# Optimization experiments

Measured on AMD Instinct MI355X. Metric: run time of the kernel, lower is better.

## Reference

```python
import jax, jax.numpy as jnp
import numpy as np

# Per-chromosome bin counts: round(len/100000) for hg38 chromosome lengths (from __init__)
CHROM_BINS = [2490, 2422, 1983, 1902, 1815, 1708, 1593, 1451, 1384, 1338, 1351,
              1333, 1144, 1070, 1020, 903, 833, 804, 586, 644, 467, 508]
LOC = np.concatenate([[0], np.cumsum(CHROM_BINS)])  # 23 boundaries, LOC[-1] == 28749
TOTAL_BINS = int(LOC[-1])
COMP = 50          # compression_size
N_HEADS = 22
INPUT_DIM = N_HEADS * COMP * 2  # 2200
H1, H2, OUT = 1000, 50, 13
BATCH = 2048


def setup_inputs() -> dict:
    key = jax.random.key(0)
    ks = jax.random.split(key, 12)
    s = 0.02
    return {
        "input_tensor": jax.random.normal(ks[0], (BATCH, 2, TOTAL_BINS), jnp.float32),
        # all 22 head weight matrices concatenated along the input dim: (COMP, TOTAL_BINS)
        "head_w": jax.random.normal(ks[1], (COMP, TOTAL_BINS), jnp.float32) * s,
        "head_b": jax.random.normal(ks[2], (N_HEADS, COMP), jnp.float32) * s,
        "conc_w": jax.random.normal(ks[3], (INPUT_DIM, INPUT_DIM), jnp.float32) * s,
        "conc_b": jax.random.normal(ks[4], (INPUT_DIM,), jnp.float32) * s,
        "w1": jax.random.normal(ks[5], (H1, INPUT_DIM), jnp.float32) * s,
        "b1": jax.random.normal(ks[6], (H1,), jnp.float32) * s,
        "w2": jax.random.normal(ks[7], (H2, H1), jnp.float32) * s,
        "b2": jax.random.normal(ks[8], (H2,), jnp.float32) * s,
        "w3": jax.random.normal(ks[9], (OUT, H2), jnp.float32) * s,
        "b3": jax.random.normal(ks[10], (OUT,), jnp.float32) * s,
    }


def reference(input_tensor, head_w, head_b, conc_w, conc_b, w1, b1, w2, b2, w3, b3):
    # 22 per-chromosome heads, each applied to both channels; output order per
    # chromosome i is [head_i(ch0), head_i(ch1)], matching the torch loop.
    pieces = []
    for i in range(N_HEADS):
        a, b = int(LOC[i]), int(LOC[i + 1])
        seg = input_tensor[:, :, a:b]                       # (B, 2, L_i)
        h = jnp.einsum('bcl,ol->bco', seg, head_w[:, a:b]) + head_b[i]  # (B, 2, COMP)
        pieces.append(h.reshape(h.shape[0], -1))            # (B, 2*COMP)
    combined = jnp.concatenate(pieces, axis=1)              # (B, 2200)
    z = combined @ conc_w.T + conc_b                        # conc Linear
    # seq: Linear -> Dropout(eval=id) -> LeakyReLU -> Linear -> Dropout -> LeakyReLU -> Dropout -> Linear
    h1 = jax.nn.leaky_relu(z @ w1.T + b1, 0.01)
    h2 = jax.nn.leaky_relu(h1 @ w2.T + b2, 0.01)
    return h2 @ w3.T + b3                                   # (B, 13)
```

## Files before the change

kernel.cpp:

```cpp
#include <hip/hip_runtime.h>
#include <cstdint>

typedef __bf16 bf16_t;
typedef __bf16 bf16x4 __attribute__((ext_vector_type(4)));
typedef __bf16 bf16x8 __attribute__((ext_vector_type(8)));
typedef float  f32x4  __attribute__((ext_vector_type(4)));
typedef float  f32x4u __attribute__((ext_vector_type(4), aligned(4)));

#define TOTAL_BINS 28749
#define WH_LD64    29312
#define N_HEADS    22
#define BATCH      2048
#define ROWS       4096
#define IDIM       2200
#define IDIM_P     2208
#define IDIM_NP    2240
#define H1DIM      1000
#define H1_NP      1024
#define H2DIM      50
#define ODIM       13
#define KSPLIT     8

__constant__ int d_LOC[23]  = {0,2490,4912,6895,8797,10612,12320,13913,15364,16748,
                               18086,19437,20770,21914,22984,24004,24907,25740,26544,
                               27130,27774,28241,28749};
__constant__ int d_HA64[23] = {0,2496,4928,6912,8832,10688,12416,14016,15488,16896,
                               18240,19648,20992,22144,23232,24256,25216,26112,26944,
                               27584,28288,28800,29312};

__device__ __forceinline__ void g2lds16(const void* g, void* l) {
  __builtin_amdgcn_global_load_lds((const __attribute__((address_space(1))) void*)g,
                                   (__attribute__((address_space(3))) void*)l, 16, 0, 0);
}

__device__ __forceinline__ f32x4 mfma16(bf16x8 a, bf16x8 b, f32x4 c) {
  return __builtin_amdgcn_mfma_f32_16x16x32_bf16(a, b, c, 0, 0, 0);
}

__global__ __launch_bounds__(256) void convert_pad8(const float* __restrict__ src,
                                                    bf16_t* __restrict__ dst,
                                                    int rows, int cols, int prow, int pcol)
{
  size_t i = (size_t)blockIdx.x * 256 + threadIdx.x;
  int pc8 = pcol >> 3;
  if (i >= (size_t)prow * pc8) return;
  int r  = (int)(i / pc8);
  int c0 = (int)(i - (size_t)r * pc8) * 8;
  bf16x8 o;
  if (r < rows && c0 + 8 <= cols) {
    f32x4u a = *(const f32x4u*)(src + (size_t)r * cols + c0);
    f32x4u b = *(const f32x4u*)(src + (size_t)r * cols + c0 + 4);
    #pragma unroll
    for (int j = 0; j < 4; j++) { o[j] = (bf16_t)a[j]; o[4 + j] = (bf16_t)b[j]; }
  } else {
    #pragma unroll
    for (int j = 0; j < 8; j++) {
      int c = c0 + j;
      o[j] = (bf16_t)((r < rows && c < cols) ? src[(size_t)r * cols + c] : 0.0f);
    }
  }
  *(bf16x8*)(dst + (size_t)r * pcol + c0) = o;
}

__global__ __launch_bounds__(256) void convert_headw8(const float* __restrict__ src,
                                                      bf16_t* __restrict__ dst)
{
  size_t i = (size_t)blockIdx.x * 256 + threadIdx.x;
  const int pc8 = WH_LD64 / 8;
  if (i >= (size_t)64 * pc8) return;
  int r  = (int)(i / pc8);
  int c0 = (int)(i - (size_t)r * pc8) * 8;
  int head = 0;
  #pragma unroll
  for (int h = 0; h < N_HEADS; h++) if (c0 >= d_HA64[h + 1]) head = h + 1;
  const int ha = d_HA64[head], a = d_LOC[head];
  const int L  = d_LOC[head + 1] - a;
  const int k0 = c0 - ha;
  bf16x8 o;
  if (r < 50 && k0 + 8 <= L) {
    const float* s = src + (size_t)r * TOTAL_BINS + a + k0;
    f32x4u x = *(const f32x4u*)(s);
    f32x4u y = *(const f32x4u*)(s + 4);
    #pragma unroll
    for (int j = 0; j < 4; j++) { o[j] = (bf16_t)x[j]; o[4 + j] = (bf16_t)y[j]; }
  } else {
    #pragma unroll
    for (int j = 0; j < 8; j++) {
      int k = k0 + j;
      o[j] = (bf16_t)((r < 50 && k < L) ? src[(size_t)r * TOTAL_BINS + a + k] : 0.0f);
    }
  }
  *(bf16x8*)(dst + (size_t)r * WH_LD64 + c0) = o;
}

__global__ __launch_bounds__(256) void head_gemm2(const float* __restrict__ X,
                                                  const bf16_t* __restrict__ Wh,
                                                  const float* __restrict__ headb,
                                                  bf16_t* __restrict__ Cmb)
{
  __shared__ __attribute__((aligned(16))) bf16_t Ws[2][64][72];
  const int tid = threadIdx.x, lane = tid & 63, wid = tid >> 6;
  const int head = blockIdx.y;
  const int a   = d_LOC[head];
  const int ha  = d_HA64[head];
  const int L64 = d_HA64[head + 1] - ha;
  const int m0  = blockIdx.x * 64;
  const int la = lane & 15, lk = lane >> 4;
  const int wrow = m0 + wid * 16 + la;
  const uint32_t rowbase = (uint32_t)wrow * TOTAL_BINS + (uint32_t)a;
  const uint32_t MAX4 = (uint32_t)ROWS * TOTAL_BINS - 4;

  const int sn = tid >> 2, skg = (tid & 3) * 16;
  const bf16_t* wsrc = Wh + (size_t)sn * WH_LD64 + ha + skg;

  f32x4 acc[4] = {};

  #define LOADA(dst, kbase) do {                                     \
    uint32_t b0_ = (kbase) + (uint32_t)(lk * 8);                     \
    dst[0] = *(const f32x4u*)(X + min(b0_,      MAX4));              \
    dst[1] = *(const f32x4u*)(X + min(b0_ + 4,  MAX4));              \
    dst[2] = *(const f32x4u*)(X + min(b0_ + 32, MAX4));              \
    dst[3] = *(const f32x4u*)(X + min(b0_ + 36, MAX4));              \
  } while (0)

  {
    uint4 w0 = *(const uint4*)(wsrc);
    uint4 w1 = *(const uint4*)(wsrc + 8);
    *(uint4*)(&Ws[0][sn][skg])     = w0;
    *(uint4*)(&Ws[0][sn][skg + 8]) = w1;
  }
  f32x4u ar[4];
  LOADA(ar, rowbase);

  const int nIter = L64 >> 6;
  for (int i = 0; i < nIter; i++) {
    __syncthreads();
    const int cur = i & 1, nxt = cur ^ 1;
    uint4 nw0, nw1; f32x4u an[4];
    const bool more = (i + 1 < nIter);
    if (more) {
      const bf16_t* ws2 = wsrc + (size_t)(i + 1) * 64;
      nw0 = *(const uint4*)(ws2);
      nw1 = *(const uint4*)(ws2 + 8);
      LOADA(an, rowbase + (uint32_t)(i + 1) * 64);
    }
    bf16x8 af[2];
    #pragma unroll
    for (int kq = 0; kq < 2; kq++)
      #pragma unroll
      for (int j = 0; j < 8; j++)
        af[kq][j] = (bf16_t)ar[kq * 2 + (j >> 2)][j & 3];
    #pragma unroll
    for (int kq = 0; kq < 2; kq++)
      #pragma unroll
      for (int j = 0; j < 4; j++) {
        bf16x8 bf = *(const bf16x8*)(&Ws[cur][j * 16 + la][kq * 32 + lk * 8]);
        acc[j] = mfma16(af[kq], bf, acc[j]);
      }
    if (more) {
      *(uint4*)(&Ws[nxt][sn][skg])     = nw0;
      *(uint4*)(&Ws[nxt][sn][skg + 8]) = nw1;
      #pragma unroll
      for (int q = 0; q < 4; q++) ar[q] = an[q];
    }
  }

  #pragma unroll
  for (int j = 0; j < 4; j++) {
    int o = j * 16 + la;
    if (o < 50) {
      float bv = headb[head * 50 + o];
      #pragma unroll
      for (int r = 0; r < 4; r++) {
        int gr = m0 + wid * 16 + lk * 4 + r;
        Cmb[(size_t)(gr >> 1) * IDIM_P + head * 100 + (gr & 1) * 50 + o] =
            (bf16_t)(acc[j][r] + bv);
      }
    }
  }
  #undef LOADA
}

__global__ __launch_bounds__(256) void gemm_bt64(const bf16_t* __restrict__ A, int lda,
                                                 const bf16_t* __restrict__ W, int ldb,
                                                 const float* __restrict__ bias,
                                                 void* __restrict__ Cout, int ldc,
                                                 int K, int N, int act, int out_f32)
{
  __shared__ __attribute__((aligned(16))) bf16_t As[2][128][32];
  __shared__ __attribute__((aligned(16))) bf16_t Bs[2][64][32];
  const int tid  = threadIdx.x;
  const int lane = tid & 63, wid = tid >> 6;
  const int m0 = blockIdx.x * 128;
  const int n0 = blockIdx.y * 64;
  const int la = lane & 15, lk = lane >> 4;
  const int wm = wid * 32;
  const int scg = (((tid & 3) ^ ((tid >> 3) & 3)) * 8);
  const int lks = ((lk ^ ((la >> 1) & 3)) * 8);

  f32x4 acc[2][4] = {};

  const bf16_t* asrc0 = A + (size_t)(m0 + (tid >> 2)) * lda + scg;
  const bf16_t* asrc1 = asrc0 + (size_t)64 * lda;
  const bf16_t* wsrc  = W + (size_t)(n0 + (tid >> 2)) * ldb + scg;

  auto stage = [&](int buf, int k0) {
    g2lds16(asrc0 + k0, &As[buf][0][0] + tid * 8);
    g2lds16(asrc1 + k0, &As[buf][64][0] + tid * 8);
    g2lds16(wsrc  + k0, &Bs[buf][0][0] + tid * 8);
  };
  stage(0, 0);

  int i = 0;
  for (int k0 = 0; k0 < K; k0 += 32, i++) {
    __syncthreads();
    const int cur = i & 1;
    if (k0 + 32 < K) stage(cur ^ 1, k0 + 32);
    bf16x8 af[2], bfr[4];
    #pragma unroll
    for (int ii = 0; ii < 2; ii++) af[ii]  = *(const bf16x8*)(&As[cur][wm + ii * 16 + la][lks]);
    #pragma unroll
    for (int j = 0; j < 4; j++)    bfr[j] = *(const bf16x8*)(&Bs[cur][j * 16 + la][lks]);
    #pragma unroll
    for (int ii = 0; ii < 2; ii++)
      #pragma unroll
      for (int j = 0; j < 4; j++)
        acc[ii][j] = mfma16(af[ii], bfr[j], acc[ii][j]);
  }

  float bv[4]; bool ok[4]; int gcv[4];
  #pragma unroll
  for (int j = 0; j < 4; j++) {
    int gc = n0 + j * 16 + la;
    gcv[j] = gc; ok[j] = gc < N;
    bv[j] = ok[j] ? bias[gc] : 0.0f;
  }
  #pragma unroll
  for (int ii = 0; ii < 2; ii++) {
    #pragma unroll
    for (int r = 0; r < 4; r++) {
      int gr = m0 + wm + ii * 16 + lk * 4 + r;
      #pragma unroll
      for (int j = 0; j < 4; j++) {
        if (ok[j]) {
          float v = acc[ii][j][r] + bv[j];
          if (act) v = fmaxf(v, 0.01f * v);
          if (out_f32) ((float*) Cout)[(size_t)gr * ldc + gcv[j]] = v;
          else         ((bf16_t*)Cout)[(size_t)gr * ldc + gcv[j]] = (bf16_t)v;
        }
      }
    }
  }
}

__global__ __launch_bounds__(256) void gemm_splitk(const bf16_t* __restrict__ A,
                                                   const bf16_t* __restrict__ W,
                                                   float* __restrict__ P)
{
  __shared__ __attribute__((aligned(16))) bf16_t As[2][128][32];
  __shared__ __attribute__((aligned(16))) bf16_t Bs[2][64][32];
  const int tid  = threadIdx.x;
  const int lane = tid & 63, wid = tid >> 6;
  const int m0 = blockIdx.x * 128;
  const int split = blockIdx.y;
  const int kb = split * (H1_NP / KSPLIT);
  const int la = lane & 15, lk = lane >> 4;
  const int wm = wid * 32;
  const int scg = (((tid & 3) ^ ((tid >> 3) & 3)) * 8);
  const int lks = ((lk ^ ((la >> 1) & 3)) * 8);

  f32x4 acc[2][4] = {};

  const bf16_t* asrc0 = A + (size_t)(m0 + (tid >> 2)) * H1_NP + kb + scg;
  const bf16_t* asrc1 = asrc0 + (size_t)64 * H1_NP;
  const bf16_t* wsrc  = W + (size_t)(tid >> 2) * H1_NP + kb + scg;

  auto stage = [&](int buf, int k0) {
    g2lds16(asrc0 + k0, &As[buf][0][0] + tid * 8);
    g2lds16(asrc1 + k0, &As[buf][64][0] + tid * 8);
    g2lds16(wsrc  + k0, &Bs[buf][0][0] + tid * 8);
  };
  stage(0, 0);

  #pragma unroll
  for (int i = 0; i < 4; i++) {
    __syncthreads();
    const int cur = i & 1;
    if (i < 3) stage(cur ^ 1, (i + 1) * 32);
    bf16x8 af[2], bfr[4];
    #pragma unroll
    for (int ii = 0; ii < 2; ii++) af[ii]  = *(const bf16x8*)(&As[cur][wm + ii * 16 + la][lks]);
    #pragma unroll
    for (int j = 0; j < 4; j++)    bfr[j] = *(const bf16x8*)(&Bs[cur][j * 16 + la][lks]);
    #pragma unroll
    for (int ii = 0; ii < 2; ii++)
      #pragma unroll
      for (int j = 0; j < 4; j++)
        acc[ii][j] = mfma16(af[ii], bfr[j], acc[ii][j]);
  }

  #pragma unroll
  for (int ii = 0; ii < 2; ii++)
    #pragma unroll
    for (int r = 0; r < 4; r++) {
      int gr = m0 + wm + ii * 16 + lk * 4 + r;
      #pragma unroll
      for (int j = 0; j < 4; j++)
        P[((size_t)split * BATCH + gr) * 64 + j * 16 + la] = acc[ii][j][r];
    }
}

__global__ __launch_bounds__(256) void finalize_tail(const float* __restrict__ P,
                                                     const float* __restrict__ b2,
                                                     const float* __restrict__ w3,
                                                     const float* __restrict__ b3,
                                                     float* __restrict__ out)
{
  __shared__ float h2s[16][64];
  const int r0 = blockIdx.x * 16;
  const int t = threadIdx.x;
  const int r = t >> 4, c4 = (t & 15) * 4;
  f32x4 s = {};
  #pragma unroll
  for (int sp = 0; sp < KSPLIT; sp++) {
    const f32x4 v = *(const f32x4*)(P + ((size_t)sp * BATCH + r0 + r) * 64 + c4);
    s.x += v.x; s.y += v.y; s.z += v.z; s.w += v.w;
  }
  #pragma unroll
  for (int c = 0; c < 4; c++) {
    int col = c4 + c;
    float v = s[c] + ((col < H2DIM) ? b2[col] : 0.0f);
    h2s[r][col] = fmaxf(v, 0.01f * v);
  }
  __syncthreads();
  if (t < 16 * ODIM) {
    int rr = t / ODIM, o = t - rr * ODIM;
    float acc = b3[o];
    #pragma unroll 10
    for (int k = 0; k < H2DIM; k++) acc += h2s[rr][k] * w3[o * H2DIM + k];
    out[(size_t)(r0 + rr) * ODIM + o] = acc;
  }
}

extern "C" void kernel_launch(void* const* d_in, const int* in_sizes, int n_in,
                              void* d_out, int out_size, void* d_ws, size_t ws_size,
                              hipStream_t stream)
{
  const float* X      = (const float*)d_in[0];
  const float* head_w = (const float*)d_in[1];
  const float* head_b = (const float*)d_in[2];
  const float* conc_w = (const float*)d_in[3];
  const float* conc_b = (const float*)d_in[4];
  const float* w1     = (const float*)d_in[5];
  const float* b1     = (const float*)d_in[6];
  const float* w2     = (const float*)d_in[7];
  const float* b2     = (const float*)d_in[8];
  const float* w3     = (const float*)d_in[9];
  const float* b3     = (const float*)d_in[10];

  char* p = (char*)d_ws;
  auto alloc = [&](size_t bytes) { char* r = p; p += (bytes + 255) & ~(size_t)255; return r; };
  bf16_t* headw_ws = (bf16_t*)alloc((size_t)64 * WH_LD64 * 2);
  bf16_t* concw_ws = (bf16_t*)alloc((size_t)IDIM_NP * IDIM_P * 2);
  bf16_t* w1_ws    = (bf16_t*)alloc((size_t)H1_NP * IDIM_P * 2);
  bf16_t* w2_ws    = (bf16_t*)alloc((size_t)128 * H1_NP * 2);
  bf16_t* comb     = (bf16_t*)alloc((size_t)BATCH * IDIM_P * 2);
  bf16_t* zbuf     = (bf16_t*)alloc((size_t)BATCH * IDIM_P * 2);
  bf16_t* h1buf    = (bf16_t*)alloc((size_t)BATCH * H1_NP * 2);
  float*  h2p      = (float*) alloc((size_t)KSPLIT * BATCH * 64 * 4);

  auto cgrid = [](size_t n) { return dim3((unsigned)((n + 255) / 256)); };

  convert_headw8<<<cgrid((size_t)64 * WH_LD64 / 8), 256, 0, stream>>>(head_w, headw_ws);
  convert_pad8<<<cgrid((size_t)IDIM_NP * IDIM_P / 8), 256, 0, stream>>>(conc_w, concw_ws, IDIM, IDIM, IDIM_NP, IDIM_P);
  convert_pad8<<<cgrid((size_t)H1_NP * IDIM_P / 8), 256, 0, stream>>>(w1, w1_ws, H1DIM, IDIM, H1_NP, IDIM_P);
  convert_pad8<<<cgrid((size_t)128 * H1_NP / 8), 256, 0, stream>>>(w2, w2_ws, H2DIM, H1DIM, 128, H1_NP);

  head_gemm2<<<dim3(ROWS / 64, N_HEADS), 256, 0, stream>>>(X, headw_ws, head_b, comb);

  gemm_bt64<<<dim3(BATCH / 128, IDIM_NP / 64), 256, 0, stream>>>(
      comb, IDIM_P, concw_ws, IDIM_P, conc_b, zbuf, IDIM_P, IDIM_P, IDIM, 0, 0);
  gemm_bt64<<<dim3(BATCH / 128, H1_NP / 64), 256, 0, stream>>>(
      zbuf, IDIM_P, w1_ws, IDIM_P, b1, h1buf, H1_NP, IDIM_P, H1DIM, 1, 0);

  gemm_splitk<<<dim3(BATCH / 128, KSPLIT), 256, 0, stream>>>(h1buf, w2_ws, h2p);
  finalize_tail<<<dim3(BATCH / 16), 256, 0, stream>>>(h2p, b2, w3, b3, (float*)d_out);
}
```

Before: 801.7 us.

## Fuse weight conversions, split-K the w1 GEMM, and remap workgroups across XCDs

Merges the four weight-conversion launches into one kernel that dispatches on block index, which cuts launch overhead. The w1 GEMM, which had only 256 blocks, now runs as a two-way split-K writing fp32 partials, and a new reduce kernel sums them and applies bias and LeakyReLU. Both GEMMs also remap the linear block index in an 8-way interleave, apparently to group tiles per XCD for better L2 locality. The trade is extra fp32 partial traffic, about 16MB written and read, and one more launch.

```diff
diff --git a/kernel.cpp b/kernel.cpp
--- a/kernel.cpp
+++ b/kernel.cpp
@@ -20,6 +20,13 @@
 #define H2DIM      50
 #define ODIM       13
 #define KSPLIT     8
+#define KCH_W1     1120
+
+#define NB_HW  916
+#define NB_CW  2415
+#define NB_W1  1104
+#define NB_W2  64
+#define NB_ALL (NB_HW + NB_CW + NB_W1 + NB_W2)
 
 __constant__ int d_LOC[23]  = {0,2490,4912,6895,8797,10612,12320,13913,15364,16748,
                                18086,19437,20770,21914,22984,24004,24907,25740,26544,
@@ -37,60 +44,74 @@
   return __builtin_amdgcn_mfma_f32_16x16x32_bf16(a, b, c, 0, 0, 0);
 }
 
-__global__ __launch_bounds__(256) void convert_pad8(const float* __restrict__ src,
-                                                    bf16_t* __restrict__ dst,
-                                                    int rows, int cols, int prow, int pcol)
-{
-  size_t i = (size_t)blockIdx.x * 256 + threadIdx.x;
-  int pc8 = pcol >> 3;
-  if (i >= (size_t)prow * pc8) return;
-  int r  = (int)(i / pc8);
-  int c0 = (int)(i - (size_t)r * pc8) * 8;
+template<int RR, int CC, int PR, int PC>
+__device__ __forceinline__ void cvt_pad8_t(int i, const float* __restrict__ src,
+                                           bf16_t* __restrict__ dst)
+{
+  const int pc8 = PC >> 3;
+  int r  = i / pc8;
+  int c0 = (i - r * pc8) * 8;
   bf16x8 o;
-  if (r < rows && c0 + 8 <= cols) {
-    f32x4u a = *(const f32x4u*)(src + (size_t)r * cols + c0);
-    f32x4u b = *(const f32x4u*)(src + (size_t)r * cols + c0 + 4);
+  if (r < RR && c0 + 8 <= CC) {
+    f32x4u a = *(const f32x4u*)(src + (size_t)r * CC + c0);
+    f32x4u b = *(const f32x4u*)(src + (size_t)r * CC + c0 + 4);
     #pragma unroll
     for (int j = 0; j < 4; j++) { o[j] = (bf16_t)a[j]; o[4 + j] = (bf16_t)b[j]; }
   } else {
     #pragma unroll
     for (int j = 0; j < 8; j++) {
       int c = c0 + j;
-      o[j] = (bf16_t)((r < rows && c < cols) ? src[(size_t)r * cols + c] : 0.0f);
-    }
-  }
-  *(bf16x8*)(dst + (size_t)r * pcol + c0) = o;
-}
-
-__global__ __launch_bounds__(256) void convert_headw8(const float* __restrict__ src,
-                                                      bf16_t* __restrict__ dst)
-{
-  size_t i = (size_t)blockIdx.x * 256 + threadIdx.x;
-  const int pc8 = WH_LD64 / 8;
-  if (i >= (size_t)64 * pc8) return;
-  int r  = (int)(i / pc8);
-  int c0 = (int)(i - (size_t)r * pc8) * 8;
-  int head = 0;
-  #pragma unroll
-  for (int h = 0; h < N_HEADS; h++) if (c0 >= d_HA64[h + 1]) head = h + 1;
-  const int ha = d_HA64[head], a = d_LOC[head];
-  const int L  = d_LOC[head + 1] - a;
-  const int k0 = c0 - ha;
-  bf16x8 o;
-  if (r < 50 && k0 + 8 <= L) {
-    const float* s = src + (size_t)r * TOTAL_BINS + a + k0;
-    f32x4u x = *(const f32x4u*)(s);
-    f32x4u y = *(const f32x4u*)(s + 4);
-    #pragma unroll
-    for (int j = 0; j < 4; j++) { o[j] = (bf16_t)x[j]; o[4 + j] = (bf16_t)y[j]; }
-  } else {
-    #pragma unroll
-    for (int j = 0; j < 8; j++) {
-      int k = k0 + j;
-      o[j] = (bf16_t)((r < 50 && k < L) ? src[(size_t)r * TOTAL_BINS + a + k] : 0.0f);
-    }
-  }
-  *(bf16x8*)(dst + (size_t)r * WH_LD64 + c0) = o;
+      o[j] = (bf16_t)((r < RR && c < CC) ? src[(size_t)r * CC + c] : 0.0f);
+    }
+  }
+  *(bf16x8*)(dst + (size_t)r * PC + c0) = o;
+}
+
+__global__ __launch_bounds__(256) void convert_all(const float* __restrict__ head_w,
+                                                   const float* __restrict__ conc_w,
+                                                   const float* __restrict__ w1,
+                                                   const float* __restrict__ w2,
+                                                   bf16_t* __restrict__ headw_ws,
+                                                   bf16_t* __restrict__ concw_ws,
+                                                   bf16_t* __restrict__ w1_ws,
+                                                   bf16_t* __restrict__ w2_ws)
+{
+  int b = blockIdx.x;
+  const int t = threadIdx.x;
+  if (b < NB_HW) {
+    int i  = b * 256 + t;
+    const int pc8 = WH_LD64 / 8;
+    int r  = i / pc8;
+    int c0 = (i - r * pc8) * 8;
+    int head = 0;
+    #pragma unroll
+    for (int h = 0; h < N_HEADS; h++) if (c0 >= d_HA64[h + 1]) head = h + 1;
+    const int ha = d_HA64[head], a = d_LOC[head];
+    const int L  = d_LOC[head + 1] - a;
+    const int k0 = c0 - ha;
+    bf16x8 o;
+    if (r < 50 && k0 + 8 <= L) {
+      const float* s = head_w + (size_t)r * TOTAL_BINS + a + k0;
+      f32x4u x = *(const f32x4u*)(s);
+      f32x4u y = *(const f32x4u*)(s + 4);
+      #pragma unroll
+      for (int j = 0; j < 4; j++) { o[j] = (bf16_t)x[j]; o[4 + j] = (bf16_t)y[j]; }
+    } else {
+      #pragma unroll
+      for (int j = 0; j < 8; j++) {
+        int k = k0 + j;
+        o[j] = (bf16_t)((r < 50 && k < L) ? head_w[(size_t)r * TOTAL_BINS + a + k] : 0.0f);
+      }
+    }
+    *(bf16x8*)(headw_ws + (size_t)r * WH_LD64 + c0) = o;
+    return;
+  }
+  b -= NB_HW;
+  if (b < NB_CW) { cvt_pad8_t<IDIM, IDIM, IDIM_NP, IDIM_P>(b * 256 + t, conc_w, concw_ws); return; }
+  b -= NB_CW;
+  if (b < NB_W1) { cvt_pad8_t<H1DIM, IDIM, H1_NP, IDIM_P>(b * 256 + t, w1, w1_ws); return; }
+  b -= NB_W1;
+  cvt_pad8_t<H2DIM, H1DIM, 128, H1_NP>(b * 256 + t, w2, w2_ws);
 }
 
 __global__ __launch_bounds__(256) void head_gemm2(const float* __restrict__ X,
@@ -185,14 +206,23 @@
                                                  const bf16_t* __restrict__ W, int ldb,
                                                  const float* __restrict__ bias,
                                                  void* __restrict__ Cout, int ldc,
-                                                 int K, int N, int act, int out_f32)
+                                                 int K, int KCH, int N, int act, int out_f32)
 {
   __shared__ __attribute__((aligned(16))) bf16_t As[2][128][32];
   __shared__ __attribute__((aligned(16))) bf16_t Bs[2][64][32];
   const int tid  = threadIdx.x;
   const int lane = tid & 63, wid = tid >> 6;
-  const int m0 = blockIdx.x * 128;
-  const int n0 = blockIdx.y * 64;
+
+  const int gx = gridDim.x;
+  int nwg = gx * gridDim.y;
+  int l = blockIdx.x + blockIdx.y * gx;
+  if ((nwg & 7) == 0) { int q = nwg >> 3; l = (l & 7) * q + (l >> 3); }
+  const int m0 = (l % gx) * 128;
+  const int n0 = (l / gx) * 64;
+
+  const int kb   = blockIdx.z * KCH;
+  const int klen = min(KCH, K - kb);
+
   const int la = lane & 15, lk = lane >> 4;
   const int wm = wid * 32;
   const int scg = (((tid & 3) ^ ((tid >> 3) & 3)) * 8);
@@ -200,9 +230,9 @@
 
   f32x4 acc[2][4] = {};
 
-  const bf16_t* asrc0 = A + (size_t)(m0 + (tid >> 2)) * lda + scg;
+  const bf16_t* asrc0 = A + (size_t)(m0 + (tid >> 2)) * lda + kb + scg;
   const bf16_t* asrc1 = asrc0 + (size_t)64 * lda;
-  const bf16_t* wsrc  = W + (size_t)(n0 + (tid >> 2)) * ldb + scg;
+  const bf16_t* wsrc  = W + (size_t)(n0 + (tid >> 2)) * ldb + kb + scg;
 
   auto stage = [&](int buf, int k0) {
     g2lds16(asrc0 + k0, &As[buf][0][0] + tid * 8);
@@ -212,10 +242,10 @@
   stage(0, 0);
 
   int i = 0;
-  for (int k0 = 0; k0 < K; k0 += 32, i++) {
+  for (int k0 = 0; k0 < klen; k0 += 32, i++) {
     __syncthreads();
     const int cur = i & 1;
-    if (k0 + 32 < K) stage(cur ^ 1, k0 + 32);
+    if (k0 + 32 < klen) stage(cur ^ 1, k0 + 32);
     bf16x8 af[2], bfr[4];
     #pragma unroll
     for (int ii = 0; ii < 2; ii++) af[ii]  = *(const bf16x8*)(&As[cur][wm + ii * 16 + la][lks]);
@@ -233,8 +263,9 @@
   for (int j = 0; j < 4; j++) {
     int gc = n0 + j * 16 + la;
     gcv[j] = gc; ok[j] = gc < N;
-    bv[j] = ok[j] ? bias[gc] : 0.0f;
-  }
+    bv[j] = (bias && ok[j]) ? bias[gc] : 0.0f;
+  }
+  float* Cf = (float*)Cout + (size_t)blockIdx.z * BATCH * ldc;
   #pragma unroll
   for (int ii = 0; ii < 2; ii++) {
     #pragma unroll
@@ -245,12 +276,42 @@
         if (ok[j]) {
           float v = acc[ii][j][r] + bv[j];
           if (act) v = fmaxf(v, 0.01f * v);
-          if (out_f32) ((float*) Cout)[(size_t)gr * ldc + gcv[j]] = v;
+          if (out_f32) Cf[(size_t)gr * ldc + gcv[j]] = v;
           else         ((bf16_t*)Cout)[(size_t)gr * ldc + gcv[j]] = (bf16_t)v;
         }
       }
     }
   }
+}
+
+__global__ __launch_bounds__(256) void reduce_h1(const float* __restrict__ P,
+                                                 const float* __restrict__ bias1,
+                                                 bf16_t* __restrict__ h1)
+{
+  int i  = blockIdx.x * 256 + threadIdx.x;
+  int r  = i >> 7;
+  int c0 = (i & 127) * 8;
+  const float* p0 = P + (size_t)r * H1_NP + c0;
+  const float* p1 = p0 + (size_t)BATCH * H1_NP;
+  f32x4u a0 = *(const f32x4u*)(p0),     a1 = *(const f32x4u*)(p0 + 4);
+  f32x4u c0v = *(const f32x4u*)(p1),    c1v = *(const f32x4u*)(p1 + 4);
+  float bb[8];
+  if (c0 + 8 <= H1DIM) {
+    f32x4u x = *(const f32x4u*)(bias1 + c0);
+    f32x4u y = *(const f32x4u*)(bias1 + c0 + 4);
+    #pragma unroll
+    for (int j = 0; j < 4; j++) { bb[j] = x[j]; bb[4 + j] = y[j]; }
+  } else {
+    #pragma unroll
+    for (int j = 0; j < 8; j++) { int c = c0 + j; bb[j] = (c < H1DIM) ? bias1[c] : 0.0f; }
+  }
+  bf16x8 o;
+  #pragma unroll
+  for (int j = 0; j < 4; j++) {
+    float v = a0[j] + c0v[j] + bb[j];     o[j]     = (bf16_t)fmaxf(v, 0.01f * v);
+    float w = a1[j] + c1v[j] + bb[4 + j]; o[4 + j] = (bf16_t)fmaxf(w, 0.01f * w);
+  }
+  *(bf16x8*)(h1 + (size_t)r * H1_NP + c0) = o;
 }
 
 __global__ __launch_bounds__(256) void gemm_splitk(const bf16_t* __restrict__ A,
@@ -261,8 +322,12 @@
   __shared__ __attribute__((aligned(16))) bf16_t Bs[2][64][32];
   const int tid  = threadIdx.x;
   const int lane = tid & 63, wid = tid >> 6;
-  const int m0 = blockIdx.x * 128;
-  const int split = blockIdx.y;
+
+  int l = blockIdx.x + blockIdx.y * gridDim.x;
+  { int q = (gridDim.x * gridDim.y) >> 3; l = (l & 7) * q + (l >> 3); }
+  const int m0    = (l % gridDim.x) * 128;
+  const int split = l / gridDim.x;
+
   const int kb = split * (H1_NP / KSPLIT);
   const int la = lane & 15, lk = lane >> 4;
   const int wm = wid * 32;
@@ -368,20 +433,20 @@
   bf16_t* zbuf     = (bf16_t*)alloc((size_t)BATCH * IDIM_P * 2);
   bf16_t* h1buf    = (bf16_t*)alloc((size_t)BATCH * H1_NP * 2);
   float*  h2p      = (float*) alloc((size_t)KSPLIT * BATCH * 64 * 4);
-
-  auto cgrid = [](size_t n) { return dim3((unsigned)((n + 255) / 256)); };
-
-  convert_headw8<<<cgrid((size_t)64 * WH_LD64 / 8), 256, 0, stream>>>(head_w, headw_ws);
-  convert_pad8<<<cgrid((size_t)IDIM_NP * IDIM_P / 8), 256, 0, stream>>>(conc_w, concw_ws, IDIM, IDIM, IDIM_NP, IDIM_P);
-  convert_pad8<<<cgrid((size_t)H1_NP * IDIM_P / 8), 256, 0, stream>>>(w1, w1_ws, H1DIM, IDIM, H1_NP, IDIM_P);
-  convert_pad8<<<cgrid((size_t)128 * H1_NP / 8), 256, 0, stream>>>(w2, w2_ws, H2DIM, H1DIM, 128, H1_NP);
+  float*  h1p      = (float*) alloc((size_t)2 * BATCH * H1_NP * 4);
+
+  convert_all<<<dim3(NB_ALL), 256, 0, stream>>>(head_w, conc_w, w1, w2,
+                                                headw_ws, concw_ws, w1_ws, w2_ws);
 
   head_gemm2<<<dim3(ROWS / 64, N_HEADS), 256, 0, stream>>>(X, headw_ws, head_b, comb);
 
-  gemm_bt64<<<dim3(BATCH / 128, IDIM_NP / 64), 256, 0, stream>>>(
-      comb, IDIM_P, concw_ws, IDIM_P, conc_b, zbuf, IDIM_P, IDIM_P, IDIM, 0, 0);
-  gemm_bt64<<<dim3(BATCH / 128, H1_NP / 64), 256, 0, stream>>>(
-      zbuf, IDIM_P, w1_ws, IDIM_P, b1, h1buf, H1_NP, IDIM_P, H1DIM, 1, 0);
+  gemm_bt64<<<dim3(BATCH / 128, IDIM_NP / 64, 1), 256, 0, stream>>>(
+      comb, IDIM_P, concw_ws, IDIM_P, conc_b, zbuf, IDIM_P, IDIM_P, IDIM_P, IDIM, 0, 0);
+
+  gemm_bt64<<<dim3(BATCH / 128, H1_NP / 64, 2), 256, 0, stream>>>(
+      zbuf, IDIM_P, w1_ws, IDIM_P, nullptr, h1p, H1_NP, IDIM_P, KCH_W1, H1_NP, 0, 1);
+
+  reduce_h1<<<dim3(BATCH * H1_NP / 8 / 256), 256, 0, stream>>>(h1p, b1, h1buf);
 
   gemm_splitk<<<dim3(BATCH / 128, KSPLIT), 256, 0, stream>>>(h1buf, w2_ws, h2p);
   finalize_tail<<<dim3(BATCH / 16), 256, 0, stream>>>(h2p, b2, w3, b3, (float*)d_out);
```

Result: faster. 771.7 us (-3.7%).
